# Kernel tuning notes

Hardware: AMD Instinct MI355X
Metric: run time of the kernel (lower is better)

Reference implementation:

```python
import jax, jax.numpy as jnp
import numpy as np

B, T, D, L, S = 128, 96, 800, 128, 10  # batch, time, features, latent, MC samples (hard-coded 10 in source)
LOG2PI = float(np.log(2.0 * np.pi))
RAW_SIGMA_BIAS = 0.5


def _linear_params(key, out_dim, in_dim):
    s = 1.0 / np.sqrt(in_dim)
    kw, kb = jax.random.split(key)
    W = jax.random.uniform(kw, (out_dim, in_dim), minval=-s, maxval=s, dtype=jnp.float32)
    b = jax.random.uniform(kb, (out_dim,), minval=-s, maxval=s, dtype=jnp.float32)
    return W, b


def setup_inputs() -> dict:
    key = jax.random.key(0)
    ks = jax.random.split(key, 12)
    W_px, b_px = _linear_params(ks[0], L, D)        # phi_x
    W_pz, b_pz = _linear_params(ks[1], L, L)        # phi_z
    W_pr, b_pr = _linear_params(ks[2], 2 * L, L)    # prior
    W_en, b_en = _linear_params(ks[3], 2 * L, 2 * L)  # encoder
    W_de, b_de = _linear_params(ks[4], D, 2 * L)    # decoder
    s = 1.0 / np.sqrt(L)
    W_ih = jax.random.uniform(ks[5], (4 * L, 2 * L), minval=-s, maxval=s, dtype=jnp.float32)
    W_hh = jax.random.uniform(ks[6], (4 * L, L), minval=-s, maxval=s, dtype=jnp.float32)
    b_ih = jax.random.uniform(ks[7], (4 * L,), minval=-s, maxval=s, dtype=jnp.float32)
    b_hh = jax.random.uniform(ks[8], (4 * L,), minval=-s, maxval=s, dtype=jnp.float32)
    inputs = jax.random.uniform(ks[9], (B, T, D), dtype=jnp.float32)  # four-hot-ish data in [0,1]
    eps = jax.random.normal(ks[10], (T, B, S, L), dtype=jnp.float32)  # reparameterization noise
    beta = jnp.ones((1,), jnp.float32)
    return dict(inputs=inputs, beta=beta, eps=eps, W_px=W_px, b_px=b_px, W_pz=W_pz, b_pz=b_pz,
                W_pr=W_pr, b_pr=b_pr, W_en=W_en, b_en=b_en, W_de=W_de, b_de=b_de,
                W_ih=W_ih, W_hh=W_hh, b_ih=b_ih, b_hh=b_hh)


def _vrnn_loss(inputs, beta, eps, W_px, b_px, W_pz, b_pz, W_pr, b_pr, W_en, b_en, W_de, b_de, W_ih, W_hh, b_ih, b_hh):
    Bsz, Tlen, _ = inputs.shape
    Lat = W_px.shape[0]
    mean_ = jnp.float32(0.0)  # self.mean logit offset
    b_lstm = b_ih + b_hh

    def lstm_step(carry, x_s):
        h, c = carry
        gates = x_s @ W_ih.T + h @ W_hh.T + b_lstm  # [B, 4L], torch gate order i,f,g,o
        i, f, g, o = jnp.split(gates, 4, axis=-1)
        c = jax.nn.sigmoid(f) * c + jax.nn.sigmoid(i) * jnp.tanh(g)
        h = jax.nn.sigmoid(o) * jnp.tanh(c)
        return (h, c), h

    def step(carry, xs):
        out, h, c = carry
        x, eps_t = xs  # [B,D], [B,S,L]
        x_hat = jax.nn.relu(x @ W_px.T + b_px)  # [B,L]
        # prior
        ph = jax.nn.relu(out @ W_pr.T + b_pr)
        mu_p, ls_p = jnp.split(ph, 2, axis=-1)
        sigma_p = jnp.maximum(jax.nn.softplus(jnp.exp(ls_p) + RAW_SIGMA_BIAS), 0.0)
        # posterior (mu shifted by prior mu)
        eh = jax.nn.relu(jnp.concatenate([out, x_hat], axis=-1) @ W_en.T + b_en)
        mu_q, ls_q = jnp.split(eh, 2, axis=-1)
        mu_q = mu_q + mu_p
        sigma_q = jnp.exp(ls_q)
        # 10-way reparameterized sampling
        z = mu_q[:, None, :] + sigma_q[:, None, :] * eps_t  # [B,S,L]
        z_hat = jax.nn.relu(z @ W_pz.T + b_pz)  # [B,S,L]
        out_b = jnp.broadcast_to(out[:, None, :], z_hat.shape)
        logits = jax.nn.relu(jnp.concatenate([z_hat, out_b], axis=-1) @ W_de.T + b_de) + mean_  # [B,S,D]
        # Bernoulli log-prob: x*l - softplus(l), summed over features
        log_px = jnp.sum(logits * x[:, None, :] - jax.nn.softplus(logits), axis=-1)  # [B,S]
        log_pz = jnp.sum(-0.5 * jnp.square((z - mu_p[:, None, :]) / sigma_p[:, None, :])
                         - jnp.log(sigma_p)[:, None, :] - 0.5 * LOG2PI, axis=-1)  # [B,S]
        log_qz = jnp.sum(-0.5 * jnp.square((z - mu_q[:, None, :]) / sigma_q[:, None, :])
                         - jnp.log(sigma_q)[:, None, :] - 0.5 * LOG2PI, axis=-1)  # [B,S]
        kl = log_qz - log_pz
        elbo = jnp.mean(log_px - beta * kl, axis=-1)  # [B], MC average over S samples
        # LSTM over the S samples as a length-S sequence (as in the source)
        rnn_in = jnp.concatenate([jnp.broadcast_to(x_hat[:, None, :], z_hat.shape), z_hat], axis=-1)  # [B,S,2L]
        (h, c), outs = jax.lax.scan(lstm_step, (h, c), jnp.swapaxes(rnn_in, 0, 1))  # outs [S,B,L]
        out_new = jnp.mean(outs, axis=0)  # [B,L] (mean over samples, matching h_out semantics)
        return (out_new, h, c), elbo

    zeros = jnp.zeros((Bsz, Lat), inputs.dtype)
    xs = (jnp.swapaxes(inputs, 0, 1), eps)  # time-major
    _, elbos = jax.lax.scan(step, (zeros, zeros, zeros), xs)  # [T,B]
    return -jnp.mean(jnp.sum(elbos, axis=0) / Tlen)


def reference(inputs, beta, eps, W_px, b_px, W_pz, b_pz, W_pr, b_pr, W_en, b_en, W_de, b_de, W_ih, W_hh, b_ih, b_hh):
    return _vrnn_loss(inputs, beta, eps, W_px, b_px, W_pz, b_pz, W_pr, b_pr,
                      W_en, b_en, W_de, b_de, W_ih, W_hh, b_ih, b_hh)
```

## Files before the change

kernel.cpp:

```cpp
#include <hip/hip_runtime.h>
#include <math.h>

#define TT 96
#define BB 128
#define DD 800
#define LL 128

typedef _Float16 h2v __attribute__((ext_vector_type(2)));
typedef _Float16 f16x8 __attribute__((ext_vector_type(8)));
typedef float f32x4 __attribute__((ext_vector_type(4)));

constexpr size_t O_WPX   = 0;
constexpr size_t O_WPR   = O_WPX   + 102400;
constexpr size_t O_WEN   = O_WPR   + 16384;
constexpr size_t O_BFENX = O_WEN   + 32768;
constexpr size_t O_BFIZ  = O_BFENX + 16384;
constexpr size_t O_BFHH  = O_BFIZ  + 32768;
constexpr size_t O_BFDE  = O_BFHH  + 32768;
constexpr size_t O_BFPZ  = O_BFDE  + 102400;
constexpr size_t O_BL    = O_BFPZ  + 8192;
constexpr size_t O_ACC   = O_BL    + 512;
constexpr size_t O_PROG  = O_ACC   + 4;
constexpr size_t O_XHAT  = O_PROG  + 128;
constexpr size_t O_GX    = O_XHAT  + 786432;
constexpr size_t O_ENCX  = O_GX    + 6291456;
constexpr size_t O_OUT   = O_ENCX  + 3145728;
constexpr size_t O_Q2    = O_OUT   + 1572864;
constexpr size_t O_P2    = O_Q2    + 3145728;

__device__ __forceinline__ h2v u2h(unsigned u) {
  union { unsigned u; h2v h; } x; x.u = u; return x.h;
}
__device__ __forceinline__ float fdot2(unsigned w, unsigned v, float acc) {
  return __builtin_amdgcn_fdot2(u2h(w), u2h(v), acc, false);
}
__device__ __forceinline__ unsigned packf16(float a, float b) {
  union { _Float16 h[2]; unsigned u; } x;
  x.h[0] = (_Float16)a; x.h[1] = (_Float16)b;
  return x.u;
}
__device__ __forceinline__ f16x8 u4h8(uint4 u) {
  union { uint4 u; f16x8 h; } x; x.u = u; return x.h;
}
__device__ __forceinline__ f32x4 mfma16(uint4 a, uint4 b, f32x4 c) {
  return __builtin_amdgcn_mfma_f32_16x16x32_f16(u4h8(a), u4h8(b), c, 0, 0, 0);
}
__device__ __forceinline__ float frcp(float x) { return __builtin_amdgcn_rcpf(x); }
__device__ __forceinline__ float fsigm(float x) { return frcp(1.f + __expf(-x)); }
__device__ __forceinline__ float ftanh(float x) {
  float e = __expf(2.f * fabsf(x));
  float t = 1.f - 2.f * frcp(e + 1.f);
  return copysignf(t, x);
}
__device__ __forceinline__ float hsum4(float4 a) { return (a.x + a.y) + (a.z + a.w); }

__device__ __forceinline__ void dotacc4(uint4 wv, uint4 vv, float4& av) {
  av.x = fdot2(wv.x, vv.x, av.x);
  av.y = fdot2(wv.y, vv.y, av.y);
  av.z = fdot2(wv.z, vv.z, av.z);
  av.w = fdot2(wv.w, vv.w, av.w);
}

__device__ __forceinline__ void bar_lds() {
  asm volatile("s_waitcnt lgkmcnt(0)" ::: "memory");
  __builtin_amdgcn_sched_barrier(0);
  __builtin_amdgcn_s_barrier();
  __builtin_amdgcn_sched_barrier(0);
}

__device__ __forceinline__ void gstore(float* p, float v) {
  __hip_atomic_store(p, v, __ATOMIC_RELAXED, __HIP_MEMORY_SCOPE_AGENT);
}
__device__ __forceinline__ float gload(const float* p) {
  return __hip_atomic_load(p, __ATOMIC_RELAXED, __HIP_MEMORY_SCOPE_AGENT);
}
__device__ __forceinline__ void gstore2(float2* p, float a, float b) {
  union { float f[2]; unsigned long long u; } x; x.f[0] = a; x.f[1] = b;
  __hip_atomic_store((unsigned long long*)p, x.u, __ATOMIC_RELAXED, __HIP_MEMORY_SCOPE_AGENT);
}
__device__ __forceinline__ float2 gload2(const float2* p) {
  unsigned long long u = __hip_atomic_load((const unsigned long long*)p,
                                           __ATOMIC_RELAXED, __HIP_MEMORY_SCOPE_AGENT);
  union { unsigned long long u; float2 f; } x; x.u = u; return x.f;
}

__device__ __forceinline__ int swz128(int row, int col) {
  return row * 128 + (col ^ ((row & 7) << 3));
}
__device__ __forceinline__ int swz256(int row, int col) {
  return row * 256 + (col ^ ((row & 7) << 3));
}

__global__ void prep_misc(const float* __restrict__ b_ih, const float* __restrict__ b_hh,
                          float* __restrict__ b_lstm, double* __restrict__ accum,
                          int* __restrict__ prog) {
  int t = threadIdx.x;
  if (t < 512) b_lstm[t] = b_ih[t] + b_hh[t];
  if (t == 0) accum[0] = 0.0;
  if (t < 128) __hip_atomic_store(&prog[t], 0, __ATOMIC_RELAXED, __HIP_MEMORY_SCOPE_AGENT);
}

__global__ void prep_pack_f16(const float* __restrict__ src, unsigned* __restrict__ dst,
                              int J, int rs, int k0, int total) {
  int idx = blockIdx.x * 256 + threadIdx.x;
  if (idx >= total) return;
  int u = idx & 3;
  int t2 = idx >> 2;
  int k8 = t2 / J;
  int j = t2 - k8 * J;
  int k = k8 * 8 + u * 2;
  const float* r = src + (size_t)j * rs + k0 + k;
  dst[idx] = packf16(r[0], r[1]);
}

__global__ void prep_bfrag(const float* __restrict__ src, unsigned* __restrict__ dst,
                           int rs, int k0, int KS, int mode, int total) {
  int idx = blockIdx.x * 256 + threadIdx.x;
  if (idx >= total) return;
  int jj = idx & 3;
  int lane = (idx >> 2) & 63;
  int t2 = idx >> 8;
  int ks = t2 % KS;
  int g = t2 / KS;
  int n = (mode == 0) ? (128 * (g & 3) + 16 * (g >> 2) + (lane & 15))
                      : (16 * g + (lane & 15));
  int k = ks * 32 + (lane >> 4) * 8 + jj * 2;
  const float* r = src + (size_t)n * rs + k0 + k;
  dst[idx] = packf16(r[0], r[1]);
}

__global__ void prep_transpose(const float* __restrict__ src, float* __restrict__ dst,
                               int J, int rs, int k0, int total) {
  int idx = blockIdx.x * 256 + threadIdx.x;
  if (idx >= total) return;
  int J4 = J * 4;
  int k4 = idx / J4;
  int rem = idx - k4 * J4;
  int j = rem >> 2;
  int kk = rem & 3;
  dst[idx] = src[j * rs + k0 + k4 * 4 + kk];
}

__device__ __forceinline__ float dot4(float4 w, float4 v) {
  return w.x*v.x + w.y*v.y + w.z*v.z + w.w*v.w;
}
__global__ __launch_bounds__(256) void xhat_kernel(const float* __restrict__ x,
                                                   const float* __restrict__ Wpx4,
                                                   const float* __restrict__ b_px,
                                                   unsigned* __restrict__ xhat2) {
  __shared__ __align__(16) float sx[8][800];
  const int wg = blockIdx.x, tid = threadIdx.x;
  const int p0 = wg * 8;
  for (int r = 0; r < 8; ++r) {
    int p = p0 + r; int t = p >> 7; int b = p & 127;
    const float* row = x + ((size_t)b * TT + t) * 800;
    for (int col = tid; col < 800; col += 256) sx[r][col] = row[col];
  }
  __syncthreads();
  const int j = tid & 127, g = tid >> 7;
  float acc[4];
  const float bj = b_px[j];
  #pragma unroll
  for (int u = 0; u < 4; ++u) acc[u] = bj;
  const float4* W = (const float4*)Wpx4;
  #pragma unroll 2
  for (int k4 = 0; k4 < 200; ++k4) {
    float4 w = W[k4 * 128 + j];
    #pragma unroll
    for (int u = 0; u < 4; ++u) {
      float4 xv = *(const float4*)&sx[g + 2*u][k4 * 4];
      acc[u] += dot4(w, xv);
    }
  }
  #pragma unroll
  for (int u = 0; u < 4; ++u) {
    float v = fmaxf(acc[u], 0.f);
    float vp = __shfl_xor(v, 1, 64);
    if ((j & 1) == 0) {
      int p = p0 + g + 2*u;
      xhat2[(size_t)p * 64 + (j >> 1)] = packf16(v, vp);
    }
  }
}

__global__ __launch_bounds__(512) void prep_gx(
    const unsigned* __restrict__ xhat2, const uint4* __restrict__ BFihz,
    const float* __restrict__ b_lstm, float* __restrict__ gxh) {
  const int tid = threadIdx.x;
  const int wv = tid >> 6, lane = tid & 63, l15 = lane & 15, quad = lane >> 4;
  const int p0 = blockIdx.x * 16;
  uint4 a[4];
  #pragma unroll
  for (int ks = 0; ks < 4; ++ks)
    a[ks] = *(const uint4*)&xhat2[(size_t)(p0 + l15) * 64 + ks * 16 + quad * 4];
  #pragma unroll
  for (int nt = 0; nt < 4; ++nt) {
    int g = wv * 4 + nt;
    int n = 128 * (g & 3) + 16 * (g >> 2) + l15;
    float bl = b_lstm[n];
    f32x4 acc = {0.f, 0.f, 0.f, 0.f};
    #pragma unroll
    for (int ks = 0; ks < 4; ++ks)
      acc = mfma16(a[ks], BFihz[(g * 4 + ks) * 64 + lane], acc);
    #pragma unroll
    for (int r = 0; r < 4; ++r)
      gxh[(size_t)(p0 + quad * 4 + r) * 512 + n] = acc[r] + bl;
  }
}

__global__ __launch_bounds__(512) void prep_encx(
    const unsigned* __restrict__ xhat2, const uint4* __restrict__ BFenx,
    float* __restrict__ encx) {
  const int tid = threadIdx.x;
  const int wv = tid >> 6, lane = tid & 63, l15 = lane & 15, quad = lane >> 4;
  const int p0 = blockIdx.x * 16;
  uint4 a[4];
  #pragma unroll
  for (int ks = 0; ks < 4; ++ks)
    a[ks] = *(const uint4*)&xhat2[(size_t)(p0 + l15) * 64 + ks * 16 + quad * 4];
  #pragma unroll
  for (int gt = 0; gt < 2; ++gt) {
    int g = wv * 2 + gt;
    f32x4 acc = {0.f, 0.f, 0.f, 0.f};
    #pragma unroll
    for (int ks = 0; ks < 4; ++ks)
      acc = mfma16(a[ks], BFenx[(g * 4 + ks) * 64 + lane], acc);
    #pragma unroll
    for (int r = 0; r < 4; ++r)
      encx[(size_t)(p0 + quad * 4 + r) * 256 + 16 * g + l15] = acc[r];
  }
}

__global__ __launch_bounds__(512) void fused_kernel(
    const float* __restrict__ eps,
    const uint4* __restrict__ Wpr4, const float* __restrict__ b_pr,
    const uint4* __restrict__ Wen4, const float* __restrict__ b_en,
    const uint4* __restrict__ BFpz, const float* __restrict__ b_pz,
    const uint4* __restrict__ BFihz, const uint4* __restrict__ BFhh,
    const float* __restrict__ gxh_g, const float* __restrict__ encx_g,
    float* __restrict__ g_out, float2* __restrict__ g_q2, float2* __restrict__ g_p2,
    const float* __restrict__ x, const float* __restrict__ beta_p,
    const uint4* __restrict__ BFde, const float* __restrict__ b_de,
    double* __restrict__ accum, int* __restrict__ prog)
{
  __shared__ __align__(16) char SMEM[161536];
  const int tid = threadIdx.x;

  if (blockIdx.x < 128) {
    float* s_gz       = (float*)SMEM;
    float* s_ehmu     = (float*)SMEM;
    float* s_mup      = (float*)(SMEM + 512);
    float* s_sgp      = (float*)(SMEM + 1024);
    float* s_sgq      = (float*)(SMEM + 1536);
    _Float16* s_z2    = (_Float16*)(SMEM + 20480);
    _Float16* s_zh2   = (_Float16*)(SMEM + 24832);
    float* s_out      = (float*)(SMEM + 29184);
    unsigned* s_out2  = (unsigned*)(SMEM + 29696);
    _Float16* s_h2    = (_Float16*)(SMEM + 29952);
    uint4* s_bfihz    = (uint4*)(SMEM + 30464);

    const int b = blockIdx.x;
    const int wv = tid >> 6;
    const int lane = tid & 63;
    const int l15 = lane & 15;
    const int quad = lane >> 4;

    #pragma unroll
    for (int i = 0; i < 16; ++i)
      s_bfihz[i * 512 + tid] = BFihz[i * 512 + tid];

    if (tid < 128) { s_out[tid] = 0.f; s_h2[tid] = (_Float16)0.f; }
    if (tid < 64) s_out2[tid] = 0u;
    float c_reg = 0.f;
    const float bias_pe = (tid < 256) ? b_pr[tid] : b_en[tid - 256];
    const float bz = b_pz[16 * wv + l15];
    const int gxoff = 16 * wv + l15;

    uint4 whhf[16], bfpz[4];
    #pragma unroll
    for (int i = 0; i < 16; ++i) whhf[i] = BFhh[(wv * 16 + i) * 64 + lane];
    #pragma unroll
    for (int ks = 0; ks < 4; ++ks) bfpz[ks] = BFpz[(wv * 4 + ks) * 64 + lane];

    __syncthreads();

    for (int t = 0; t < TT; ++t) {
      const size_t pb = (size_t)t * BB + b;
      const float* epsb = eps + pb * 1280;
      float e0 = epsb[tid];
      float e1 = epsb[tid + 512];
      float e2 = (tid < 256) ? epsb[tid + 1024] : 0.f;
      float gxf[4];
      #pragma unroll
      for (int nt = 0; nt < 4; ++nt)
        gxf[nt] = gxh_g[pb * 512 + 128 * nt + gxoff];
      float encx_r = (tid >= 256) ? encx_g[pb * 256 + (tid - 256)] : 0.f;

      {
        float4 a4 = {bias_pe, 0.f, 0.f, 0.f};
        if (tid < 256) {
          #pragma unroll 4
          for (int k8 = 0; k8 < 16; ++k8) {
            uint4 w = Wpr4[k8 * 256 + tid];
            uint4 o = *(const uint4*)&s_out2[k8 * 4];
            dotacc4(w, o, a4);
          }
          float ph = fmaxf(hsum4(a4), 0.f);
          if (tid < 128) s_mup[tid] = ph;
          else {
            float y = __expf(ph) + 0.5f;
            float sp = (y > 20.f) ? y : __logf(1.f + __expf(y));
            s_sgp[tid - 128] = sp;
          }
        } else {
          int j2 = tid - 256;
          #pragma unroll 4
          for (int k8 = 0; k8 < 16; ++k8) {
            uint4 w = Wen4[k8 * 256 + j2];
            uint4 o = *(const uint4*)&s_out2[k8 * 4];
            dotacc4(w, o, a4);
          }
          float eh = fmaxf(hsum4(a4) + encx_r, 0.f);
          if (j2 < 128) s_ehmu[j2] = eh;
          else s_sgq[j2 - 128] = __expf(eh);
        }
      }
      bar_lds();

      {
        int l = tid & 127, s0 = tid >> 7;
        float mu = s_ehmu[l] + s_mup[l];
        float sq = s_sgq[l];
        s_z2[s0 * 136 + l]        = (_Float16)(mu + sq * e0);
        s_z2[(s0 + 4) * 136 + l]  = (_Float16)(mu + sq * e1);
        if (tid < 256) s_z2[(s0 + 8) * 136 + l] = (_Float16)(mu + sq * e2);
      }
      bar_lds();

      if (tid < 128) {
        gstore2(&g_q2[pb * 128 + tid], s_ehmu[tid] + s_mup[tid], s_sgq[tid]);
      } else if (tid < 256) {
        gstore(&g_out[pb * 128 + tid - 128], s_out[tid - 128]);
      } else if (tid < 384) {
        int l = tid - 256;
        gstore2(&g_p2[pb * 128 + l], s_mup[l], s_sgp[l]);
      }

      {
        uint4 a[4];
        #pragma unroll
        for (int ks = 0; ks < 4; ++ks)
          a[ks] = *(const uint4*)&s_z2[l15 * 136 + ks * 32 + quad * 8];
        f32x4 acc = {bz, bz, bz, bz};
        #pragma unroll
        for (int ks = 0; ks < 4; ++ks)
          acc = mfma16(a[ks], bfpz[ks], acc);
        #pragma unroll
        for (int r = 0; r < 4; ++r) {
          int s = quad * 4 + r;
          if (s < 10)
            s_zh2[s * 136 + 16 * wv + l15] = (_Float16)fmaxf(acc[r], 0.f);
        }
      }
      bar_lds();

      {
        uint4 a[4];
        #pragma unroll
        for (int ks = 0; ks < 4; ++ks)
          a[ks] = *(const uint4*)&s_zh2[l15 * 136 + ks * 32 + quad * 8];
        #pragma unroll
        for (int nt = 0; nt < 4; ++nt) {
          float gx = gxf[nt];
          f32x4 acc = {gx, gx, gx, gx};
          #pragma unroll
          for (int ks = 0; ks < 4; ++ks)
            acc = mfma16(a[ks], s_bfihz[((wv * 4 + nt) * 4 + ks) * 64 + lane], acc);
          #pragma unroll
          for (int r = 0; r < 4; ++r) {
            int s = quad * 4 + r;
            if (s < 10)
              s_gz[s * 512 + 128 * nt + 16 * wv + l15] = acc[r];
          }
        }
      }
      __syncthreads();

      if (tid == 0)
        __hip_atomic_store(&prog[b], t + 1, __ATOMIC_RELAXED, __HIP_MEMORY_SCOPE_AGENT);

      float oacc = 0.f;
      for (int s = 0; s < 10; ++s) {
        const _Float16* hb = &s_h2[(s & 1) * 128];
        uint4 a[4];
        #pragma unroll
        for (int ks = 0; ks < 4; ++ks)
          a[ks] = *(const uint4*)&hb[ks * 32 + quad * 8];
        f32x4 acc[4];
        #pragma unroll
        for (int nt = 0; nt < 4; ++nt) {
          float cz = s_gz[s * 512 + 128 * nt + 16 * wv + l15];
          acc[nt] = f32x4{cz, cz, cz, cz};
        }
        #pragma unroll
        for (int nt = 0; nt < 4; ++nt)
          #pragma unroll
          for (int ks = 0; ks < 4; ++ks)
            acc[nt] = mfma16(a[ks], whhf[nt * 4 + ks], acc[nt]);
        if (lane < 16) {
          float gi = acc[0][0], gf = acc[1][0], gg = acc[2][0], go = acc[3][0];
          c_reg = fsigm(gf) * c_reg + fsigm(gi) * ftanh(gg);
          float h = fsigm(go) * ftanh(c_reg);
          oacc += h;
          s_h2[((s + 1) & 1) * 128 + 16 * wv + lane] = (_Float16)h;
        }
        if (s < 9) bar_lds();
      }
      if (lane < 16) {
        float v = oacc * 0.1f;
        s_out[16 * wv + lane] = v;
        float vn = __shfl_xor(v, 1, 64);
        if (!(lane & 1)) s_out2[8 * wv + (lane >> 1)] = packf16(v, vn);
      }
      bar_lds();
    }
  } else {
    _Float16* c_z2   = (_Float16*)SMEM;
    _Float16* c_a2   = (_Float16*)(SMEM + 12288);
    float* c_x       = (float*)(SMEM + 36864);
    unsigned* c_out2 = (unsigned*)(SMEM + 49664);
    float* c_muq     = (float*)(SMEM + 50688);
    float* c_sgq     = (float*)(SMEM + 52736);
    float* c_mup     = (float*)(SMEM + 54784);
    float* c_sgp     = (float*)(SMEM + 56832);
    float* c_wred    = (float*)(SMEM + 58880);

    const int cid = blockIdx.x - 128;
    const int wv = tid >> 6;
    const int lane = tid & 63;
    const int l15 = lane & 15;
    const int quad = lane >> 4;
    const float beta = beta_p[0];

    for (int c = cid; c < 3072; c += 128) {
      const int p0 = c * 4;
      const int t = p0 >> 7;
      const int b0 = p0 & 127;

      if (tid < 4) {
        while (__hip_atomic_load(&prog[b0 + tid], __ATOMIC_RELAXED,
                                 __HIP_MEMORY_SCOPE_AGENT) <= t)
          __builtin_amdgcn_s_sleep(8);
      }
      __syncthreads();

      float acc_loc = 0.f;
      {
        size_t gi = (size_t)p0 * 128 + tid;
        float2 q = gload2(&g_q2[gi]); c_muq[tid] = q.x; c_sgq[tid] = q.y;
        float2 pv = gload2(&g_p2[gi]); c_mup[tid] = pv.x; c_sgp[tid] = pv.y;
      }
      if (tid < 256) {
        int pair = tid >> 6, m = tid & 63;
        const float* o = g_out + (size_t)p0 * 128 + pair * 128;
        c_out2[tid] = packf16(gload(o + 2*m), gload(o + 2*m + 1));
      }
      for (int i = tid; i < 3200; i += 512) {
        int pp = i / 800;
        int d = i - pp * 800;
        int p = p0 + pp, bb = p & 127, tt2 = p >> 7;
        c_x[i] = x[((size_t)bb * TT + tt2) * 800 + d];
      }
      __syncthreads();

      {
        int l = tid & 127, pp = tid >> 7;
        float mq = c_muq[pp*128 + l], sq = c_sgq[pp*128 + l];
        float mp = c_mup[pp*128 + l], spv = c_sgp[pp*128 + l];
        float inv_sp = frcp(spv);
        float lsq = __logf(sq), lsp = __logf(spv);
        const float* ep = eps + (size_t)(p0 + pp) * 1280 + l;
        float kl = 0.f;
        #pragma unroll
        for (int s = 0; s < 10; ++s) {
          float e = ep[s * 128];
          float z = mq + sq * e;
          c_z2[swz128(pp * 10 + s, l)] = (_Float16)z;
          float ap = (z - mp) * inv_sp;
          kl += (-0.5f * e * e - lsq) - (-0.5f * ap * ap - lsp);
        }
        acc_loc -= beta * kl;
      }
      for (int i = tid; i < 2560; i += 512) {
        int r = i >> 6, m = i & 63;
        int pp = (r * 205) >> 11;
        ((unsigned*)c_a2)[r * 128 + 64 + (m ^ ((r & 7) << 2))] = c_out2[pp * 64 + m];
      }
      __syncthreads();

      for (int tile = wv; tile < 24; tile += 8) {
        int mt = tile >> 3, nt = tile & 7;
        uint4 a[4];
        #pragma unroll
        for (int ks = 0; ks < 4; ++ks)
          a[ks] = *(const uint4*)&c_z2[swz128(mt * 16 + l15, ks * 32 + quad * 8)];
        float bzt = b_pz[16 * nt + l15];
        f32x4 acc = {bzt, bzt, bzt, bzt};
        #pragma unroll
        for (int ks = 0; ks < 4; ++ks)
          acc = mfma16(a[ks], BFpz[(nt * 4 + ks) * 64 + lane], acc);
        #pragma unroll
        for (int r = 0; r < 4; ++r) {
          int row = mt * 16 + quad * 4 + r;
          c_a2[swz256(row, 16 * nt + l15)] = (_Float16)fmaxf(acc[r], 0.f);
        }
      }
      __syncthreads();

      #pragma unroll
      for (int mt = 0; mt < 3; ++mt) {
        uint4 a[8];
        #pragma unroll
        for (int ks = 0; ks < 8; ++ks)
          a[ks] = *(const uint4*)&c_a2[swz256(mt * 16 + l15, ks * 32 + quad * 8)];
        for (int nt = wv; nt < 50; nt += 8) {
          f32x4 acc = {0.f, 0.f, 0.f, 0.f};
          #pragma unroll
          for (int ks = 0; ks < 8; ++ks)
            acc = mfma16(a[ks], BFde[(nt * 8 + ks) * 64 + lane], acc);
          int d = 16 * nt + l15;
          float bd = b_de[d];
          #pragma unroll
          for (int r = 0; r < 4; ++r) {
            int row = mt * 16 + quad * 4 + r;
            if (row < 40) {
              int pp = (row * 205) >> 11;
              float lg = fmaxf(acc[r] + bd, 0.f);
              float xd = c_x[pp * 800 + d];
              acc_loc += xd * lg - lg - __logf(1.f + __expf(-lg));
            }
          }
        }
      }

      float v = acc_loc;
      #pragma unroll
      for (int off = 32; off > 0; off >>= 1) v += __shfl_down(v, off, 64);
      if ((tid & 63) == 0) c_wred[tid >> 6] = v;
      __syncthreads();
      if (tid == 0) {
        double tot = 0.0;
        #pragma unroll
        for (int w = 0; w < 8; ++w) tot += (double)c_wred[w];
        atomicAdd(accum, tot);
      }
      __syncthreads();
    }
  }
}

__global__ void finalize_kernel(const double* __restrict__ accum, float* __restrict__ out) {
  if (threadIdx.x == 0 && blockIdx.x == 0)
    out[0] = (float)(-accum[0] / 122880.0);
}

extern "C" void kernel_launch(void* const* d_in, const int* in_sizes, int n_in,
                              void* d_out, int out_size, void* d_ws, size_t ws_size,
                              hipStream_t stream) {
  const float* x    = (const float*)d_in[0];
  const float* beta = (const float*)d_in[1];
  const float* eps  = (const float*)d_in[2];
  const float* W_px = (const float*)d_in[3];
  const float* b_px = (const float*)d_in[4];
  const float* W_pz = (const float*)d_in[5];
  const float* b_pz = (const float*)d_in[6];
  const float* W_pr = (const float*)d_in[7];
  const float* b_pr = (const float*)d_in[8];
  const float* W_en = (const float*)d_in[9];
  const float* b_en = (const float*)d_in[10];
  const float* W_de = (const float*)d_in[11];
  const float* b_de = (const float*)d_in[12];
  const float* W_ih = (const float*)d_in[13];
  const float* W_hh = (const float*)d_in[14];
  const float* b_ih = (const float*)d_in[15];
  const float* b_hh = (const float*)d_in[16];
  float* ws = (float*)d_ws;

  prep_misc<<<dim3(1), dim3(512), 0, stream>>>(b_ih, b_hh, ws + O_BL,
                                               (double*)(ws + O_ACC), (int*)(ws + O_PROG));

  auto pk = [&](const float* src, size_t off, int J, int rs, int k0, int K) {
    int total = J * (K / 2);
    prep_pack_f16<<<dim3((total + 255) / 256), dim3(256), 0, stream>>>(
        src, (unsigned*)(ws + off), J, rs, k0, total);
  };
  pk(W_pr, O_WPR, 256, 128, 0, 128);
  pk(W_en, O_WEN, 256, 256, 0, 128);
  prep_bfrag<<<dim3(64),  dim3(256), 0, stream>>>(W_en, (unsigned*)(ws + O_BFENX), 256, 128, 4, 1, 16384);
  prep_bfrag<<<dim3(128), dim3(256), 0, stream>>>(W_ih, (unsigned*)(ws + O_BFIZ), 256, 128, 4, 0, 32768);
  prep_bfrag<<<dim3(128), dim3(256), 0, stream>>>(W_hh, (unsigned*)(ws + O_BFHH), 128, 0, 4, 0, 32768);
  prep_bfrag<<<dim3(32),  dim3(256), 0, stream>>>(W_pz, (unsigned*)(ws + O_BFPZ), 128, 0, 4, 1, 8192);
  prep_bfrag<<<dim3(400), dim3(256), 0, stream>>>(W_de, (unsigned*)(ws + O_BFDE), 256, 0, 8, 1, 102400);
  prep_transpose<<<dim3((102400 + 255) / 256), dim3(256), 0, stream>>>(
      W_px, ws + O_WPX, 128, 800, 0, 102400);

  xhat_kernel<<<dim3(1536), dim3(256), 0, stream>>>(x, ws + O_WPX, b_px, (unsigned*)(ws + O_XHAT));

  prep_gx<<<dim3(768), dim3(512), 0, stream>>>(
      (const unsigned*)(ws + O_XHAT), (const uint4*)(ws + O_BFIZ),
      ws + O_BL, ws + O_GX);
  prep_encx<<<dim3(768), dim3(512), 0, stream>>>(
      (const unsigned*)(ws + O_XHAT), (const uint4*)(ws + O_BFENX), ws + O_ENCX);

  {
    const uint4* Wpr4  = (const uint4*)(ws + O_WPR);
    const uint4* Wen4  = (const uint4*)(ws + O_WEN);
    const uint4* BFpz  = (const uint4*)(ws + O_BFPZ);
    const uint4* BFihz = (const uint4*)(ws + O_BFIZ);
    const uint4* BFhh  = (const uint4*)(ws + O_BFHH);
    const uint4* BFde  = (const uint4*)(ws + O_BFDE);
    const float* gxh   = ws + O_GX;
    const float* encx  = ws + O_ENCX;
    float* g_out = ws + O_OUT;
    float2* g_q2 = (float2*)(ws + O_Q2);
    float2* g_p2 = (float2*)(ws + O_P2);
    double* accum = (double*)(ws + O_ACC);
    int* prog = (int*)(ws + O_PROG);

    void* kargs[] = {
      (void*)&eps,
      (void*)&Wpr4, (void*)&b_pr, (void*)&Wen4, (void*)&b_en,
      (void*)&BFpz, (void*)&b_pz, (void*)&BFihz, (void*)&BFhh,
      (void*)&gxh, (void*)&encx,
      (void*)&g_out, (void*)&g_q2, (void*)&g_p2,
      (void*)&x, (void*)&beta,
      (void*)&BFde, (void*)&b_de,
      (void*)&accum, (void*)&prog
    };
    hipLaunchCooperativeKernel((void*)fused_kernel, dim3(256), dim3(512),
                               kargs, 0, stream);
  }

  finalize_kernel<<<dim3(1), dim3(64), 0, stream>>>((const double*)(ws + O_ACC), (float*)d_out);
}
```

Measured before the change: 1.050 ms.

## Merge prep kernels, widen xhat tiles, fuse gx/encx, prefetch per-step inputs

All weight packing and misc init kernels are merged into a single prep_all launch, and prep_encx is folded into prep_gx so the xhat fragments are loaded once. xhat_kernel now processes 16 rows per block instead of 8, reusing each weight load across more rows at the cost of more shared memory and registers. In the fused recurrent kernel, the eps, gx and encx loads for the next timestep are issued early, during the current step, to hide global latency on the serial path.

```diff
diff --git a/kernel.cpp b/kernel.cpp
--- a/kernel.cpp
+++ b/kernel.cpp
@@ -91,18 +91,9 @@
   return row * 256 + (col ^ ((row & 7) << 3));
 }
 
-__global__ void prep_misc(const float* __restrict__ b_ih, const float* __restrict__ b_hh,
-                          float* __restrict__ b_lstm, double* __restrict__ accum,
-                          int* __restrict__ prog) {
-  int t = threadIdx.x;
-  if (t < 512) b_lstm[t] = b_ih[t] + b_hh[t];
-  if (t == 0) accum[0] = 0.0;
-  if (t < 128) __hip_atomic_store(&prog[t], 0, __ATOMIC_RELAXED, __HIP_MEMORY_SCOPE_AGENT);
-}
-
-__global__ void prep_pack_f16(const float* __restrict__ src, unsigned* __restrict__ dst,
-                              int J, int rs, int k0, int total) {
-  int idx = blockIdx.x * 256 + threadIdx.x;
+__device__ __forceinline__ void pack_f16_body(const float* __restrict__ src,
+                                              unsigned* __restrict__ dst,
+                                              int J, int rs, int k0, int idx, int total) {
   if (idx >= total) return;
   int u = idx & 3;
   int t2 = idx >> 2;
@@ -113,9 +104,10 @@
   dst[idx] = packf16(r[0], r[1]);
 }
 
-__global__ void prep_bfrag(const float* __restrict__ src, unsigned* __restrict__ dst,
-                           int rs, int k0, int KS, int mode, int total) {
-  int idx = blockIdx.x * 256 + threadIdx.x;
+__device__ __forceinline__ void bfrag_body(const float* __restrict__ src,
+                                           unsigned* __restrict__ dst,
+                                           int rs, int k0, int KS, int mode,
+                                           int idx, int total) {
   if (idx >= total) return;
   int jj = idx & 3;
   int lane = (idx >> 2) & 63;
@@ -129,9 +121,9 @@
   dst[idx] = packf16(r[0], r[1]);
 }
 
-__global__ void prep_transpose(const float* __restrict__ src, float* __restrict__ dst,
-                               int J, int rs, int k0, int total) {
-  int idx = blockIdx.x * 256 + threadIdx.x;
+__device__ __forceinline__ void transpose_body(const float* __restrict__ src,
+                                               float* __restrict__ dst,
+                                               int J, int rs, int k0, int idx, int total) {
   if (idx >= total) return;
   int J4 = J * 4;
   int k4 = idx / J4;
@@ -141,6 +133,45 @@
   dst[idx] = src[j * rs + k0 + k4 * 4 + kk];
 }
 
+__global__ __launch_bounds__(256) void prep_all(
+    const float* __restrict__ b_ih, const float* __restrict__ b_hh,
+    const float* __restrict__ W_pr, const float* __restrict__ W_en,
+    const float* __restrict__ W_ih, const float* __restrict__ W_hh,
+    const float* __restrict__ W_pz, const float* __restrict__ W_de,
+    const float* __restrict__ W_px, float* __restrict__ ws)
+{
+  int blk = blockIdx.x;
+  const int tid = threadIdx.x;
+  if (blk < 3) {
+    if (blk < 2) {
+      int i = blk * 256 + tid;
+      ws[O_BL + i] = b_ih[i] + b_hh[i];
+    } else {
+      if (tid == 0) *(double*)(ws + O_ACC) = 0.0;
+      if (tid < 128)
+        __hip_atomic_store((int*)(ws + O_PROG) + tid, 0, __ATOMIC_RELAXED,
+                           __HIP_MEMORY_SCOPE_AGENT);
+    }
+    return;
+  }
+  blk -= 3;
+  if (blk < 64) { pack_f16_body(W_pr, (unsigned*)(ws + O_WPR), 256, 128, 0, blk * 256 + tid, 16384); return; }
+  blk -= 64;
+  if (blk < 64) { pack_f16_body(W_en, (unsigned*)(ws + O_WEN), 256, 256, 0, blk * 256 + tid, 16384); return; }
+  blk -= 64;
+  if (blk < 64) { bfrag_body(W_en, (unsigned*)(ws + O_BFENX), 256, 128, 4, 1, blk * 256 + tid, 16384); return; }
+  blk -= 64;
+  if (blk < 128) { bfrag_body(W_ih, (unsigned*)(ws + O_BFIZ), 256, 128, 4, 0, blk * 256 + tid, 32768); return; }
+  blk -= 128;
+  if (blk < 128) { bfrag_body(W_hh, (unsigned*)(ws + O_BFHH), 128, 0, 4, 0, blk * 256 + tid, 32768); return; }
+  blk -= 128;
+  if (blk < 32) { bfrag_body(W_pz, (unsigned*)(ws + O_BFPZ), 128, 0, 4, 1, blk * 256 + tid, 8192); return; }
+  blk -= 32;
+  if (blk < 400) { bfrag_body(W_de, (unsigned*)(ws + O_BFDE), 256, 0, 8, 1, blk * 256 + tid, 102400); return; }
+  blk -= 400;
+  transpose_body(W_px, ws + O_WPX, 128, 800, 0, blk * 256 + tid, 102400);
+}
+
 __device__ __forceinline__ float dot4(float4 w, float4 v) {
   return w.x*v.x + w.y*v.y + w.z*v.z + w.w*v.w;
 }
@@ -148,32 +179,32 @@
                                                    const float* __restrict__ Wpx4,
                                                    const float* __restrict__ b_px,
                                                    unsigned* __restrict__ xhat2) {
-  __shared__ __align__(16) float sx[8][800];
+  __shared__ __align__(16) float sx[16][800];
   const int wg = blockIdx.x, tid = threadIdx.x;
-  const int p0 = wg * 8;
-  for (int r = 0; r < 8; ++r) {
+  const int p0 = wg * 16;
+  for (int r = 0; r < 16; ++r) {
     int p = p0 + r; int t = p >> 7; int b = p & 127;
     const float* row = x + ((size_t)b * TT + t) * 800;
     for (int col = tid; col < 800; col += 256) sx[r][col] = row[col];
   }
   __syncthreads();
   const int j = tid & 127, g = tid >> 7;
-  float acc[4];
+  float acc[8];
   const float bj = b_px[j];
   #pragma unroll
-  for (int u = 0; u < 4; ++u) acc[u] = bj;
+  for (int u = 0; u < 8; ++u) acc[u] = bj;
   const float4* W = (const float4*)Wpx4;
   #pragma unroll 2
   for (int k4 = 0; k4 < 200; ++k4) {
     float4 w = W[k4 * 128 + j];
     #pragma unroll
-    for (int u = 0; u < 4; ++u) {
+    for (int u = 0; u < 8; ++u) {
       float4 xv = *(const float4*)&sx[g + 2*u][k4 * 4];
       acc[u] += dot4(w, xv);
     }
   }
   #pragma unroll
-  for (int u = 0; u < 4; ++u) {
+  for (int u = 0; u < 8; ++u) {
     float v = fmaxf(acc[u], 0.f);
     float vp = __shfl_xor(v, 1, 64);
     if ((j & 1) == 0) {
@@ -185,7 +216,8 @@
 
 __global__ __launch_bounds__(512) void prep_gx(
     const unsigned* __restrict__ xhat2, const uint4* __restrict__ BFihz,
-    const float* __restrict__ b_lstm, float* __restrict__ gxh) {
+    const uint4* __restrict__ BFenx, const float* __restrict__ b_lstm,
+    float* __restrict__ gxh, float* __restrict__ encx) {
   const int tid = threadIdx.x;
   const int wv = tid >> 6, lane = tid & 63, l15 = lane & 15, quad = lane >> 4;
   const int p0 = blockIdx.x * 16;
@@ -206,18 +238,6 @@
     for (int r = 0; r < 4; ++r)
       gxh[(size_t)(p0 + quad * 4 + r) * 512 + n] = acc[r] + bl;
   }
-}
-
-__global__ __launch_bounds__(512) void prep_encx(
-    const unsigned* __restrict__ xhat2, const uint4* __restrict__ BFenx,
-    float* __restrict__ encx) {
-  const int tid = threadIdx.x;
-  const int wv = tid >> 6, lane = tid & 63, l15 = lane & 15, quad = lane >> 4;
-  const int p0 = blockIdx.x * 16;
-  uint4 a[4];
-  #pragma unroll
-  for (int ks = 0; ks < 4; ++ks)
-    a[ks] = *(const uint4*)&xhat2[(size_t)(p0 + l15) * 64 + ks * 16 + quad * 4];
   #pragma unroll
   for (int gt = 0; gt < 2; ++gt) {
     int g = wv * 2 + gt;
@@ -282,19 +302,19 @@
     #pragma unroll
     for (int ks = 0; ks < 4; ++ks) bfpz[ks] = BFpz[(wv * 4 + ks) * 64 + lane];
 
+    float e0 = eps[(size_t)b * 1280 + tid];
+    float e1 = eps[(size_t)b * 1280 + tid + 512];
+    float e2 = (tid < 256) ? eps[(size_t)b * 1280 + tid + 1024] : 0.f;
+    float gxf[4];
+    #pragma unroll
+    for (int nt = 0; nt < 4; ++nt)
+      gxf[nt] = gxh_g[(size_t)b * 512 + 128 * nt + gxoff];
+    float encx_r = (tid >= 256) ? encx_g[(size_t)b * 256 + (tid - 256)] : 0.f;
+
     __syncthreads();
 
     for (int t = 0; t < TT; ++t) {
       const size_t pb = (size_t)t * BB + b;
-      const float* epsb = eps + pb * 1280;
-      float e0 = epsb[tid];
-      float e1 = epsb[tid + 512];
-      float e2 = (tid < 256) ? epsb[tid + 1024] : 0.f;
-      float gxf[4];
-      #pragma unroll
-      for (int nt = 0; nt < 4; ++nt)
-        gxf[nt] = gxh_g[pb * 512 + 128 * nt + gxoff];
-      float encx_r = (tid >= 256) ? encx_g[pb * 256 + (tid - 256)] : 0.f;
 
       {
         float4 a4 = {bias_pe, 0.f, 0.f, 0.f};
@@ -389,6 +409,17 @@
       if (tid == 0)
         __hip_atomic_store(&prog[b], t + 1, __ATOMIC_RELAXED, __HIP_MEMORY_SCOPE_AGENT);
 
+      if (t + 1 < TT) {
+        const float* epn = eps + (pb + BB) * 1280;
+        e0 = epn[tid];
+        e1 = epn[tid + 512];
+        if (tid < 256) e2 = epn[tid + 1024];
+        #pragma unroll
+        for (int nt = 0; nt < 4; ++nt)
+          gxf[nt] = gxh_g[(pb + BB) * 512 + 128 * nt + gxoff];
+        if (tid >= 256) encx_r = encx_g[(pb + BB) * 256 + (tid - 256)];
+      }
+
       float oacc = 0.f;
       for (int s = 0; s < 10; ++s) {
         const _Float16* hb = &s_h2[(s & 1) * 128];
@@ -586,31 +617,15 @@
   const float* b_hh = (const float*)d_in[16];
   float* ws = (float*)d_ws;
 
-  prep_misc<<<dim3(1), dim3(512), 0, stream>>>(b_ih, b_hh, ws + O_BL,
-                                               (double*)(ws + O_ACC), (int*)(ws + O_PROG));
-
-  auto pk = [&](const float* src, size_t off, int J, int rs, int k0, int K) {
-    int total = J * (K / 2);
-    prep_pack_f16<<<dim3((total + 255) / 256), dim3(256), 0, stream>>>(
-        src, (unsigned*)(ws + off), J, rs, k0, total);
-  };
-  pk(W_pr, O_WPR, 256, 128, 0, 128);
-  pk(W_en, O_WEN, 256, 256, 0, 128);
-  prep_bfrag<<<dim3(64),  dim3(256), 0, stream>>>(W_en, (unsigned*)(ws + O_BFENX), 256, 128, 4, 1, 16384);
-  prep_bfrag<<<dim3(128), dim3(256), 0, stream>>>(W_ih, (unsigned*)(ws + O_BFIZ), 256, 128, 4, 0, 32768);
-  prep_bfrag<<<dim3(128), dim3(256), 0, stream>>>(W_hh, (unsigned*)(ws + O_BFHH), 128, 0, 4, 0, 32768);
-  prep_bfrag<<<dim3(32),  dim3(256), 0, stream>>>(W_pz, (unsigned*)(ws + O_BFPZ), 128, 0, 4, 1, 8192);
-  prep_bfrag<<<dim3(400), dim3(256), 0, stream>>>(W_de, (unsigned*)(ws + O_BFDE), 256, 0, 8, 1, 102400);
-  prep_transpose<<<dim3((102400 + 255) / 256), dim3(256), 0, stream>>>(
-      W_px, ws + O_WPX, 128, 800, 0, 102400);
-
-  xhat_kernel<<<dim3(1536), dim3(256), 0, stream>>>(x, ws + O_WPX, b_px, (unsigned*)(ws + O_XHAT));
+  prep_all<<<dim3(1283), dim3(256), 0, stream>>>(
+      b_ih, b_hh, W_pr, W_en, W_ih, W_hh, W_pz, W_de, W_px, ws);
+
+  xhat_kernel<<<dim3(768), dim3(256), 0, stream>>>(
+      x, ws + O_WPX, b_px, (unsigned*)(ws + O_XHAT));
 
   prep_gx<<<dim3(768), dim3(512), 0, stream>>>(
       (const unsigned*)(ws + O_XHAT), (const uint4*)(ws + O_BFIZ),
-      ws + O_BL, ws + O_GX);
-  prep_encx<<<dim3(768), dim3(512), 0, stream>>>(
-      (const unsigned*)(ws + O_XHAT), (const uint4*)(ws + O_BFENX), ws + O_ENCX);
+      (const uint4*)(ws + O_BFENX), ws + O_BL, ws + O_GX, ws + O_ENCX);
 
   {
     const uint4* Wpr4  = (const uint4*)(ws + O_WPR);
```

After: 994.9 us. 5.3% less time.
